# Performance work log

Hardware: AMD Instinct MI355X
Metric: run time of the kernel (lower is better)

Reference implementation:

```python
import jax, jax.numpy as jnp
import numpy as np

B, S, H, T = 64, 512, 768, 9


def setup_inputs() -> dict:
    key = jax.random.key(0)
    ks = jax.random.split(key, 8)
    embeddings = jax.random.normal(ks[0], (B, S, H), dtype=jnp.float32)
    # variable-length mask (first token always valid), as token_type_ids would give
    lengths = jax.random.randint(ks[1], (B,), 1, S + 1)
    mask = (jnp.arange(S)[None, :] < lengths[:, None]).astype(jnp.int32)
    labels = jax.random.randint(ks[2], (B, S), 0, T)
    W = jax.random.normal(ks[3], (T, H), dtype=jnp.float32) * (1.0 / np.sqrt(H))
    b = jnp.zeros((T,), dtype=jnp.float32)
    start_trans = jax.random.normal(ks[4], (T,), dtype=jnp.float32) * 0.1
    transitions = jax.random.normal(ks[5], (T, T), dtype=jnp.float32) * 0.1
    end_trans = jax.random.normal(ks[6], (T,), dtype=jnp.float32) * 0.1
    return {"embeddings": embeddings, "W": W, "b": b,
            "start_trans": start_trans, "transitions": transitions,
            "end_trans": end_trans, "labels": labels, "mask": mask}


def _crf_nll(emissions, labels, mask_bool, start_trans, transitions, end_trans):
    # emissions: [B,S,T]; returns negative log-likelihood per sequence [B]
    Bn = emissions.shape[0]
    mask_f = mask_bool.astype(emissions.dtype)
    # --- gold path score (numerator) ---
    first = start_trans[labels[:, 0]] + emissions[jnp.arange(Bn), 0, labels[:, 0]]
    emis_sc = jnp.take_along_axis(emissions, labels[..., None], axis=2)[..., 0]  # [B,S]
    trans_sc = transitions[labels[:, :-1], labels[:, 1:]]                         # [B,S-1]
    num = first + jnp.sum((emis_sc[:, 1:] + trans_sc) * mask_f[:, 1:], axis=1)
    last_idx = jnp.sum(mask_bool.astype(jnp.int32), axis=1) - 1
    last_lab = jnp.take_along_axis(labels, last_idx[:, None], axis=1)[:, 0]
    num = num + end_trans[last_lab]
    # --- log partition (forward algorithm, logsumexp recurrence) ---
    alpha0 = start_trans[None, :] + emissions[:, 0]          # [B,T]
    em_t = jnp.swapaxes(emissions, 0, 1)[1:]                 # [S-1,B,T]
    m_t = mask_bool.T[1:]                                    # [S-1,B]
    def step(alpha, xs):
        em, m = xs
        new = jax.nn.logsumexp(alpha[:, :, None] + transitions[None], axis=1) + em
        return jnp.where(m[:, None], new, alpha), None
    alpha, _ = jax.lax.scan(step, alpha0, (em_t, m_t))
    denom = jax.nn.logsumexp(alpha + end_trans[None, :], axis=1)
    return denom - num


def reference(embeddings, W, b, start_trans, transitions, end_trans, labels, mask):
    # dropout is identity at eval; Linear + ReLU emissions
    emissions = jax.nn.relu(jnp.einsum('bsh,th->bst', embeddings, W) + b)
    # -100 padding handling: zero out mask there, clamp labels to 0
    valid = labels != -100
    mask_bool = (mask != 0) & valid
    labels_mod = jnp.where(valid, labels, 0)
    nll = _crf_nll(emissions, labels_mod, mask_bool, start_trans, transitions, end_trans)
    return jnp.mean(nll)  # == -loss.mean() of the log-likelihood
```

## Files before the change

### kernel.cpp

```cpp
#include <hip/hip_runtime.h>

#define NEG_INF (-1e30f)

static constexpr int Bn = 64;
static constexpr int Sn = 512;
static constexpr int Hn = 768;
static constexpr int Tn = 9;
static constexpr int KC = 32;
static constexpr int CL = 16;
static constexpr int PSTRIDE = 108;

__device__ __forceinline__ float dot4(float4 a, float4 b) {
    return a.x * b.x + a.y * b.y + a.z * b.z + a.w * b.w;
}

__global__ __launch_bounds__(512) void emis_kernel(const float* __restrict__ emb,
        const float* __restrict__ Wm, const float* __restrict__ bias,
        float* __restrict__ em) {
    const int blk  = blockIdx.x;
    const int tid  = threadIdx.x;
    const int lane = tid & 63;
    const int seg  = __builtin_amdgcn_readfirstlane(tid >> 6);
    const int row  = blk * 64 + lane;

    __shared__ float part[8][64][Tn];

    const float4* e4 = (const float4*)emb + (size_t)row * 192 + seg * 24;
    const float4* w4 = (const float4*)Wm;

    float acc[Tn];
#pragma unroll
    for (int t = 0; t < Tn; ++t) acc[t] = 0.0f;

#pragma unroll 4
    for (int i = 0; i < 24; ++i) {
        float4 e = e4[i];
#pragma unroll
        for (int t = 0; t < Tn; ++t) {
            float4 wt = w4[t * 192 + seg * 24 + i];
            acc[t] += dot4(e, wt);
        }
    }
#pragma unroll
    for (int t = 0; t < Tn; ++t) part[seg][lane][t] = acc[t];
    __syncthreads();

    for (int o = tid; o < 64 * Tn; o += 512) {
        int r = o / Tn, t = o - r * Tn;
        float s = 0.0f;
#pragma unroll
        for (int sg = 0; sg < 8; ++sg) s += part[sg][r][t];
        em[(size_t)blk * (64 * Tn) + o] = fmaxf(s + bias[t], 0.0f);
    }
}

__global__ __launch_bounds__(128) void chunk_kernel(const float* __restrict__ em,
        const float* __restrict__ trans, const int* __restrict__ labels,
        const int* __restrict__ mask, float* __restrict__ chunkP,
        float* __restrict__ auxN, int* __restrict__ auxC) {
    const int bk = blockIdx.x;
    const int b  = bk >> 5;
    const int k  = bk & 31;
    const int t0 = 1 + k * CL;
    const int tid  = threadIdx.x;
    const int w    = tid >> 6;
    const int lane = tid & 63;

    __shared__ float em_s[CL][Tn];
    __shared__ int   on_s[CL];
    __shared__ float tr_s[81];

    if (tid < 81) tr_s[tid] = trans[tid];

    int myLab = 0, myLabP = 0, myOn = 0;
    if (tid < CL) {
        int t = t0 + tid;
        if (t < Sn) {
            int lb = labels[b * Sn + t];
            int lp = labels[b * Sn + t - 1];
            int mm = mask[b * Sn + t];
            myOn  = (mm != 0) && (lb != -100);
            myLab = (lb == -100) ? 0 : lb;
            myLabP = (lp == -100) ? 0 : lp;
        }
        on_s[tid] = myOn;
    }
    {
        const int nst = (Sn - t0 < CL) ? (Sn - t0) : CL;
        const float* src = em + (size_t)(b * Sn + t0) * Tn;
        for (int u = tid; u < nst * Tn; u += 128) ((float*)em_s)[u] = src[u];
    }
    __syncthreads();

    float nump = 0.0f;
    int cnt = 0;
    if (tid < CL && myOn) {
        nump = em_s[tid][myLab] + tr_s[myLabP * Tn + myLab];
        cnt = 1;
    }
    if (w == 0) {
#pragma unroll
        for (int off = 8; off; off >>= 1) {
            nump += __shfl_xor(nump, off);
            cnt  += __shfl_xor(cnt, off);
        }
        if (lane == 0) { auxN[bk] = nump; auxC[bk] = cnt; }
    }

    const int v  = lane / 9;
    const int jj = lane - v * 9;
    const bool act = lane < ((w == 0) ? 45 : 36);
    const int rid = (w == 0) ? v : (5 + v);

    float c[Tn];
#pragma unroll
    for (int kk = 0; kk < Tn; ++kk) c[kk] = tr_s[kk * Tn + jj];

    float pv = (act && rid == jj) ? 0.0f : NEG_INF;

    for (int u = 0; u < CL; ++u) {
        if (!on_s[u]) continue;
        float x[Tn];
#pragma unroll
        for (int kk = 0; kk < Tn; ++kk) {
            float a = __shfl(pv, (v * Tn + kk) & 63);
            x[kk] = a + c[kk];
        }
        float mx = x[0];
#pragma unroll
        for (int kk = 1; kk < Tn; ++kk) mx = fmaxf(mx, x[kk]);
        float s = 0.0f;
#pragma unroll
        for (int kk = 0; kk < Tn; ++kk) s += __expf(x[kk] - mx);
        float nv = mx + __logf(s) + em_s[u][jj];
        pv = act ? nv : pv;
    }
    if (act) chunkP[(size_t)bk * PSTRIDE + jj * 12 + rid] = pv;
}

__global__ __launch_bounds__(64) void combine_kernel(const float* __restrict__ em,
        const float* __restrict__ startT, const float* __restrict__ endT,
        const int* __restrict__ labels, const int* __restrict__ mask,
        const float* __restrict__ chunkP, const float* __restrict__ auxN,
        const int* __restrict__ auxC, float* __restrict__ nll) {
    const int b = blockIdx.x;
    const int lane = threadIdx.x;

    float em0 = (lane < Tn) ? em[(size_t)b * Sn * Tn + lane] : NEG_INF;
    float alpha = (lane < Tn) ? (startT[lane] + em0) : NEG_INF;

    int lab0r = labels[b * Sn];
    int lab0 = (lab0r == -100) ? 0 : lab0r;
    float first = startT[lab0] + __shfl(em0, lab0);

    float numP = (lane < KC) ? auxN[b * KC + lane] : 0.0f;
    int   cntP = (lane < KC) ? auxC[b * KC + lane] : 0;
#pragma unroll
    for (int off = 32; off; off >>= 1) {
        numP += __shfl_xor(numP, off);
        cntP += __shfl_xor(cntP, off);
    }
    int m0 = ((mask[b * Sn] != 0) && (lab0r != -100)) ? 1 : 0;
    int cntTot = cntP + m0;
    int lastIdx = cntTot - 1;
    if (lastIdx < 0) lastIdx = 0;
    int lastLab = labels[b * Sn + lastIdx];
    lastLab = (lastLab == -100) ? 0 : lastLab;
    float num = first + numP + endT[lastLab];

    const float* Pb = chunkP + (size_t)b * KC * PSTRIDE;
    float4 p0 = make_float4(0, 0, 0, 0), p1 = p0, p2 = p0;
    if (lane < Tn) {
        const float4* pp = (const float4*)(Pb + lane * 12);
        p0 = pp[0]; p1 = pp[1]; p2 = pp[2];
    }
    for (int k = 0; k < KC; ++k) {
        float4 q0 = p0, q1 = p1, q2 = p2;
        if (k + 1 < KC && lane < Tn) {
            const float4* pp = (const float4*)(Pb + (size_t)(k + 1) * PSTRIDE + lane * 12);
            p0 = pp[0]; p1 = pp[1]; p2 = pp[2];
        }
        float av[Tn];
#pragma unroll
        for (int i = 0; i < Tn; ++i) av[i] = __shfl(alpha, i);
        float x[Tn];
        x[0] = av[0] + q0.x; x[1] = av[1] + q0.y; x[2] = av[2] + q0.z;
        x[3] = av[3] + q0.w; x[4] = av[4] + q1.x; x[5] = av[5] + q1.y;
        x[6] = av[6] + q1.z; x[7] = av[7] + q1.w; x[8] = av[8] + q2.x;
        float mx = x[0];
#pragma unroll
        for (int i = 1; i < Tn; ++i) mx = fmaxf(mx, x[i]);
        float s = 0.0f;
#pragma unroll
        for (int i = 0; i < Tn; ++i) s += __expf(x[i] - mx);
        float na = mx + __logf(s);
        alpha = (lane < Tn) ? na : NEG_INF;
    }

    float z = (lane < Tn) ? (alpha + endT[lane]) : NEG_INF;
    float mx = z;
#pragma unroll
    for (int off = 32; off; off >>= 1) mx = fmaxf(mx, __shfl_xor(mx, off));
    float s = __expf(z - mx);
#pragma unroll
    for (int off = 32; off; off >>= 1) s += __shfl_xor(s, off);
    float denom = mx + __logf(s);

    if (lane == 0) nll[b] = denom - num;
}

__global__ __launch_bounds__(64) void mean_kernel(const float* __restrict__ nll,
        float* __restrict__ out) {
    float v = nll[threadIdx.x];
#pragma unroll
    for (int off = 32; off; off >>= 1) v += __shfl_xor(v, off);
    if (threadIdx.x == 0) out[0] = v * (1.0f / 64.0f);
}

extern "C" void kernel_launch(void* const* d_in, const int* in_sizes, int n_in,
                              void* d_out, int out_size, void* d_ws, size_t ws_size,
                              hipStream_t stream) {
    const float* emb    = (const float*)d_in[0];
    const float* Wm     = (const float*)d_in[1];
    const float* bias   = (const float*)d_in[2];
    const float* startT = (const float*)d_in[3];
    const float* trans  = (const float*)d_in[4];
    const float* endT   = (const float*)d_in[5];
    const int*   labels = (const int*)d_in[6];
    const int*   mask   = (const int*)d_in[7];

    float* em     = (float*)d_ws;
    float* chunkP = em + (size_t)Bn * Sn * Tn;
    float* auxN   = chunkP + (size_t)Bn * KC * PSTRIDE;
    int*   auxC   = (int*)(auxN + (size_t)Bn * KC);
    float* nll    = (float*)(auxC + (size_t)Bn * KC);
    float* out    = (float*)d_out;

    emis_kernel<<<Bn * Sn / 64, 512, 0, stream>>>(emb, Wm, bias, em);
    chunk_kernel<<<Bn * KC, 128, 0, stream>>>(em, trans, labels, mask,
                                              chunkP, auxN, auxC);
    combine_kernel<<<Bn, 64, 0, stream>>>(em, startT, endT, labels, mask,
                                          chunkP, auxN, auxC, nll);
    mean_kernel<<<1, 64, 0, stream>>>(nll, out);
}
```

Measured before the change: 60.30 us.

## Fuse emission GEMM with per-chunk CRF transfer computation in one kernel

Merges the emission projection kernel and the chunked forward-algorithm kernel so each 64-row block computes emissions into shared memory and directly runs four 16-step CRF chunks on them. This removes the global emissions buffer round-trip and one kernel launch; only row 0 emissions are written out for the combine step. The embedding loads are also restaged through padded shared tiles with register prefetch. Chunk boundaries shift by one step, which is valid because chunks still compose contiguously.

```diff
diff --git a/kernel.cpp b/kernel.cpp
--- a/kernel.cpp
+++ b/kernel.cpp
@@ -7,110 +7,132 @@
 static constexpr int Hn = 768;
 static constexpr int Tn = 9;
 static constexpr int KC = 32;
-static constexpr int CL = 16;
 static constexpr int PSTRIDE = 108;
+static constexpr int TPAD = 20;
 
 __device__ __forceinline__ float dot4(float4 a, float4 b) {
     return a.x * b.x + a.y * b.y + a.z * b.z + a.w * b.w;
 }
 
-__global__ __launch_bounds__(512) void emis_kernel(const float* __restrict__ emb,
-        const float* __restrict__ Wm, const float* __restrict__ bias,
-        float* __restrict__ em) {
+__global__ __launch_bounds__(512, 4) void fused_kernel(
+        const float* __restrict__ emb, const float* __restrict__ Wm,
+        const float* __restrict__ bias, const float* __restrict__ trans,
+        const int* __restrict__ labels, const int* __restrict__ mask,
+        float* __restrict__ chunkP, float* __restrict__ auxN,
+        int* __restrict__ auxC, float* __restrict__ emRow0) {
     const int blk  = blockIdx.x;
     const int tid  = threadIdx.x;
     const int lane = tid & 63;
     const int seg  = __builtin_amdgcn_readfirstlane(tid >> 6);
-    const int row  = blk * 64 + lane;
-
-    __shared__ float part[8][64][Tn];
-
-    const float4* e4 = (const float4*)emb + (size_t)row * 192 + seg * 24;
-    const float4* w4 = (const float4*)Wm;
+
+    __shared__ float tileU[8][64 * TPAD];
+    __shared__ float em_s[64][10];
+    __shared__ float tr_s[81];
+
+    const int rowBase = blk * 64;
+    const float4* eg = (const float4*)emb;
+
+    float4 stg[4];
+#pragma unroll
+    for (int j = 0; j < 4; ++j) {
+        int z = j * 64 + lane, r = z >> 2, c4 = z & 3;
+        stg[j] = eg[(size_t)(rowBase + r) * 192 + seg * 24 + c4];
+    }
+    if (tid < 81) tr_s[tid] = trans[tid];
+
+    float* tile = &tileU[seg][0];
+#pragma unroll
+    for (int j = 0; j < 4; ++j) {
+        int z = j * 64 + lane, r = z >> 2, c4 = z & 3;
+        *(float4*)&tile[r * TPAD + c4 * 4] = stg[j];
+    }
 
     float acc[Tn];
 #pragma unroll
     for (int t = 0; t < Tn; ++t) acc[t] = 0.0f;
 
-#pragma unroll 4
-    for (int i = 0; i < 24; ++i) {
-        float4 e = e4[i];
-#pragma unroll
-        for (int t = 0; t < Tn; ++t) {
-            float4 wt = w4[t * 192 + seg * 24 + i];
-            acc[t] += dot4(e, wt);
-        }
-    }
-#pragma unroll
-    for (int t = 0; t < Tn; ++t) part[seg][lane][t] = acc[t];
+#pragma unroll
+    for (int sb = 0; sb < 6; ++sb) {
+        float4 nst[4];
+        if (sb < 5) {
+#pragma unroll
+            for (int j = 0; j < 4; ++j) {
+                int z = j * 64 + lane, r = z >> 2, c4 = z & 3;
+                nst[j] = eg[(size_t)(rowBase + r) * 192 + seg * 24 + (sb + 1) * 4 + c4];
+            }
+        }
+#pragma unroll
+        for (int c4 = 0; c4 < 4; ++c4) {
+            float4 e = *(const float4*)&tile[lane * TPAD + c4 * 4];
+#pragma unroll
+            for (int t = 0; t < Tn; ++t) {
+                const float* wp = Wm + t * Hn + seg * 96 + sb * 16 + c4 * 4;
+                float4 wv = *(const float4*)wp;
+                acc[t] += dot4(e, wv);
+            }
+        }
+        if (sb < 5) {
+#pragma unroll
+            for (int j = 0; j < 4; ++j) {
+                int z = j * 64 + lane, r = z >> 2, c4 = z & 3;
+                *(float4*)&tile[r * TPAD + c4 * 4] = nst[j];
+            }
+        }
+    }
+
+#pragma unroll
+    for (int t = 0; t < Tn; ++t) tileU[seg][lane * Tn + t] = acc[t];
     __syncthreads();
 
     for (int o = tid; o < 64 * Tn; o += 512) {
         int r = o / Tn, t = o - r * Tn;
         float s = 0.0f;
 #pragma unroll
-        for (int sg = 0; sg < 8; ++sg) s += part[sg][r][t];
-        em[(size_t)blk * (64 * Tn) + o] = fmaxf(s + bias[t], 0.0f);
-    }
-}
-
-__global__ __launch_bounds__(128) void chunk_kernel(const float* __restrict__ em,
-        const float* __restrict__ trans, const int* __restrict__ labels,
-        const int* __restrict__ mask, float* __restrict__ chunkP,
-        float* __restrict__ auxN, int* __restrict__ auxC) {
-    const int bk = blockIdx.x;
-    const int b  = bk >> 5;
-    const int k  = bk & 31;
-    const int t0 = 1 + k * CL;
-    const int tid  = threadIdx.x;
-    const int w    = tid >> 6;
-    const int lane = tid & 63;
-
-    __shared__ float em_s[CL][Tn];
-    __shared__ int   on_s[CL];
-    __shared__ float tr_s[81];
-
-    if (tid < 81) tr_s[tid] = trans[tid];
-
-    int myLab = 0, myLabP = 0, myOn = 0;
-    if (tid < CL) {
-        int t = t0 + tid;
-        if (t < Sn) {
-            int lb = labels[b * Sn + t];
-            int lp = labels[b * Sn + t - 1];
-            int mm = mask[b * Sn + t];
-            myOn  = (mm != 0) && (lb != -100);
-            myLab = (lb == -100) ? 0 : lb;
-            myLabP = (lp == -100) ? 0 : lp;
-        }
-        on_s[tid] = myOn;
-    }
-    {
-        const int nst = (Sn - t0 < CL) ? (Sn - t0) : CL;
-        const float* src = em + (size_t)(b * Sn + t0) * Tn;
-        for (int u = tid; u < nst * Tn; u += 128) ((float*)em_s)[u] = src[u];
+        for (int sg = 0; sg < 8; ++sg) s += tileU[sg][o];
+        float v = fmaxf(s + bias[t], 0.0f);
+        em_s[r][t] = v;
+        if ((blk & 7) == 0 && r == 0) emRow0[(blk >> 3) * Tn + t] = v;
     }
     __syncthreads();
 
-    float nump = 0.0f;
-    int cnt = 0;
-    if (tid < CL && myOn) {
-        nump = em_s[tid][myLab] + tr_s[myLabP * Tn + myLab];
-        cnt = 1;
-    }
-    if (w == 0) {
+    const int w  = tid >> 6;
+    const int h  = w & 1;
+    const int cl = w >> 1;
+    const int b  = blk >> 3;
+    const int sc = (blk & 7) * 4 + cl;
+    const int s0 = (blk & 7) * 64;
+
+    const int u16 = lane & 15;
+    const int tstep = s0 + cl * 16 + u16;
+    int lb = 0, on = 0;
+    if (lane < 16) {
+        lb = labels[b * Sn + tstep];
+        int mm = mask[b * Sn + tstep];
+        on = (tstep >= 1) && (mm != 0) && (lb != -100);
+    }
+    unsigned long long bm = __ballot(on != 0);
+
+    if (h == 0) {
+        float np = 0.0f;
+        int c1 = 0;
+        if (lane < 16 && on) {
+            int lpr = labels[b * Sn + tstep - 1];
+            lpr = (lpr == -100) ? 0 : lpr;
+            np = em_s[cl * 16 + u16][lb] + tr_s[lpr * Tn + lb];
+            c1 = 1;
+        }
 #pragma unroll
         for (int off = 8; off; off >>= 1) {
-            nump += __shfl_xor(nump, off);
-            cnt  += __shfl_xor(cnt, off);
-        }
-        if (lane == 0) { auxN[bk] = nump; auxC[bk] = cnt; }
+            np += __shfl_xor(np, off);
+            c1 += __shfl_xor(c1, off);
+        }
+        if (lane == 0) { auxN[b * KC + sc] = np; auxC[b * KC + sc] = c1; }
     }
 
     const int v  = lane / 9;
     const int jj = lane - v * 9;
-    const bool act = lane < ((w == 0) ? 45 : 36);
-    const int rid = (w == 0) ? v : (5 + v);
+    const bool act = lane < (h ? 36 : 45);
+    const int rid = h ? (5 + v) : v;
 
     float c[Tn];
 #pragma unroll
@@ -118,8 +140,8 @@
 
     float pv = (act && rid == jj) ? 0.0f : NEG_INF;
 
-    for (int u = 0; u < CL; ++u) {
-        if (!on_s[u]) continue;
+    for (int u = 0; u < 16; ++u) {
+        if (!((bm >> u) & 1ull)) continue;
         float x[Tn];
 #pragma unroll
         for (int kk = 0; kk < Tn; ++kk) {
@@ -132,21 +154,22 @@
         float s = 0.0f;
 #pragma unroll
         for (int kk = 0; kk < Tn; ++kk) s += __expf(x[kk] - mx);
-        float nv = mx + __logf(s) + em_s[u][jj];
+        float nv = mx + __logf(s) + em_s[cl * 16 + u][jj];
         pv = act ? nv : pv;
     }
-    if (act) chunkP[(size_t)bk * PSTRIDE + jj * 12 + rid] = pv;
-}
-
-__global__ __launch_bounds__(64) void combine_kernel(const float* __restrict__ em,
-        const float* __restrict__ startT, const float* __restrict__ endT,
-        const int* __restrict__ labels, const int* __restrict__ mask,
-        const float* __restrict__ chunkP, const float* __restrict__ auxN,
-        const int* __restrict__ auxC, float* __restrict__ nll) {
+    if (act) chunkP[(size_t)(b * KC + sc) * PSTRIDE + jj * 12 + rid] = pv;
+}
+
+__global__ __launch_bounds__(64) void combine_kernel(
+        const float* __restrict__ emRow0, const float* __restrict__ startT,
+        const float* __restrict__ endT, const int* __restrict__ labels,
+        const int* __restrict__ mask, const float* __restrict__ chunkP,
+        const float* __restrict__ auxN, const int* __restrict__ auxC,
+        float* __restrict__ nll) {
     const int b = blockIdx.x;
     const int lane = threadIdx.x;
 
-    float em0 = (lane < Tn) ? em[(size_t)b * Sn * Tn + lane] : NEG_INF;
+    float em0 = (lane < Tn) ? emRow0[b * Tn + lane] : NEG_INF;
     float alpha = (lane < Tn) ? (startT[lane] + em0) : NEG_INF;
 
     int lab0r = labels[b * Sn];
@@ -229,17 +252,16 @@
     const int*   labels = (const int*)d_in[6];
     const int*   mask   = (const int*)d_in[7];
 
-    float* em     = (float*)d_ws;
-    float* chunkP = em + (size_t)Bn * Sn * Tn;
+    float* chunkP = (float*)d_ws;
     float* auxN   = chunkP + (size_t)Bn * KC * PSTRIDE;
     int*   auxC   = (int*)(auxN + (size_t)Bn * KC);
     float* nll    = (float*)(auxC + (size_t)Bn * KC);
+    float* emRow0 = nll + Bn;
     float* out    = (float*)d_out;
 
-    emis_kernel<<<Bn * Sn / 64, 512, 0, stream>>>(emb, Wm, bias, em);
-    chunk_kernel<<<Bn * KC, 128, 0, stream>>>(em, trans, labels, mask,
-                                              chunkP, auxN, auxC);
-    combine_kernel<<<Bn, 64, 0, stream>>>(em, startT, endT, labels, mask,
+    fused_kernel<<<512, 512, 0, stream>>>(emb, Wm, bias, trans, labels, mask,
+                                          chunkP, auxN, auxC, emRow0);
+    combine_kernel<<<Bn, 64, 0, stream>>>(emRow0, startT, endT, labels, mask,
                                           chunkP, auxN, auxC, nll);
     mean_kernel<<<1, 64, 0, stream>>>(nll, out);
 }
```

New measurement: 62.01 us. +2.8%, slower.
